# Kernel tuning notes

Hardware: AMD Instinct MI355X
Metric: run time of the kernel (lower is better)

The kernel has to match this reference:

```python
import jax, jax.numpy as jnp
import numpy as np

WS = 8
NUM_HEADS = 4
LOW_THR = 0.2
BN_EPS = 1e-5


def window_partition(x, ws):
    # x: (B, C, H, W) -> (B*nH*nW, C, ws, ws)
    B, C, H, W = x.shape
    x = x.reshape(B, C, H // ws, ws, W // ws, ws)
    return x.transpose(0, 2, 4, 1, 3, 5).reshape(-1, C, ws, ws)


def window_reverse(windows, ws, H, W):
    # (B*nH*nW, C, ws, ws) -> (B, C, H, W)
    Wn, C = windows.shape[0], windows.shape[1]
    B = Wn // ((H // ws) * (W // ws))
    x = windows.reshape(B, H // ws, W // ws, C, ws, ws)
    return x.transpose(0, 3, 1, 4, 2, 5).reshape(B, C, H, W)


def cross_attention(x1, temp, q_w, kv_w, proj_w, proj_b):
    # x1, temp: (Wn, C, h, w); per-window cross attention, windows independent.
    Wn, C, h, w = x1.shape
    N = h * w
    hd = C // NUM_HEADS
    scale = hd ** -0.5
    x1t = x1.reshape(Wn, C, N).transpose(0, 2, 1)    # (Wn, N, C)
    tt = temp.reshape(Wn, C, N).transpose(0, 2, 1)   # (Wn, N, C)
    q = (x1t @ q_w.T).reshape(Wn, N, NUM_HEADS, hd).transpose(0, 2, 1, 3)  # (Wn,H,N,hd)
    kv = (tt @ kv_w.T).reshape(Wn, N, 2, NUM_HEADS, hd).transpose(2, 0, 3, 1, 4)
    k, v = kv[0], kv[1]                               # (Wn,H,N,hd)
    attn = jax.nn.softmax(jnp.einsum('whnd,whmd->whnm', q, k) * scale, axis=-1)
    out = jnp.einsum('whnm,whmd->whnd', attn, v).transpose(0, 2, 1, 3).reshape(Wn, N, C)
    out = out @ proj_w.T + proj_b
    return out.transpose(0, 2, 1).reshape(Wn, C, h, w)


def setup_inputs() -> dict:
    key = jax.random.key(0)
    ks = jax.random.split(key, 8)
    B, C, H, W = 8, 256, 128, 128
    pre_feat = jax.random.normal(ks[0], (B, C, H, W), jnp.float32)
    feat = jax.random.normal(ks[1], (B, C, H, W), jnp.float32)
    pre_feat_mask = jnp.ones((1, 1, H, W), jnp.float32)
    feat_mask = jnp.ones((1, 1, H, W), jnp.float32)
    mask = jax.random.uniform(ks[2], (B, 1, 64, 64), jnp.float32)
    # Linear weights: torch init uses std=0.001; use small std for stable softmax.
    q_w = jax.random.normal(ks[3], (C, C), jnp.float32) * 0.02
    kv_w = jax.random.normal(ks[4], (2 * C, C), jnp.float32) * 0.02
    proj_w = jax.random.normal(ks[5], (C, C), jnp.float32) * 0.02
    proj_b = jnp.zeros((C,), jnp.float32)
    gamma = jnp.ones((C,), jnp.float32)
    beta = jnp.zeros((C,), jnp.float32)
    return {"pre_feat": pre_feat, "pre_feat_mask": pre_feat_mask, "feat": feat,
            "feat_mask": feat_mask, "mask": mask, "q_w": q_w, "kv_w": kv_w,
            "proj_w": proj_w, "proj_b": proj_b, "gamma": gamma, "beta": beta}


def reference(pre_feat, pre_feat_mask, feat, feat_mask, mask,
              q_w, kv_w, proj_w, proj_b, gamma, beta):
    B, C, H, W = feat.shape
    feat = feat * feat_mask
    pre_feat = pre_feat * pre_feat_mask
    # bilinear interpolate mask to (H, W), align_corners=False (half-pixel)
    mask = jax.image.resize(mask, (B, 1, H, W), method='bilinear')
    mask = mask * feat_mask
    feat_p = window_partition(feat, WS)          # (Wn, C, ws, ws)
    pre_p = window_partition(pre_feat, WS)
    mask_p = window_partition(mask, WS)          # (Wn, 1, ws, ws)
    Wn = mask_p.shape[0]
    mask_max = mask_p.reshape(Wn, -1).max(axis=-1)
    keep = mask_max >= LOW_THR                   # (Wn,) bool
    # Windows are independent in the per-window attention, so compute attention
    # over all windows and zero out the non-kept ones (same math as gather/scatter).
    heat_attn = cross_attention(feat_p, pre_p * mask_p, q_w, kv_w, proj_w, proj_b)
    heat_compe = jnp.where(keep[:, None, None, None], heat_attn, 0.0)
    heat_enhance = window_reverse(heat_compe, WS, H, W)
    x = heat_enhance + feat
    # training-mode BatchNorm2d with batch statistics
    mean = x.mean(axis=(0, 2, 3), keepdims=True)
    var = x.var(axis=(0, 2, 3), keepdims=True)
    xhat = (x - mean) * jax.lax.rsqrt(var + BN_EPS)
    return xhat * gamma[None, :, None, None] + beta[None, :, None, None]
```

## Files before the change

### kernel.cpp

```cpp
#include <hip/hip_runtime.h>

typedef unsigned short u16;
typedef unsigned int   u32;
typedef __attribute__((ext_vector_type(8))) short short8;
typedef __attribute__((ext_vector_type(8))) unsigned short u16x8;
typedef __attribute__((ext_vector_type(4))) float floatx4;

__device__ __forceinline__ float bf2f(u16 u) {
  union { u32 i; float f; } v; v.i = ((u32)u) << 16; return v.f;
}
__device__ __forceinline__ u16 f2bf(float f) {
  union { float f; u32 i; } v; v.f = f;
  u32 x = v.i;
  return (u16)((x + 0x7fffu + ((x >> 16) & 1u)) >> 16);
}

__device__ __forceinline__ void gl_lds16(const u16* g, u16* l) {
  __builtin_amdgcn_global_load_lds(
      (const __attribute__((address_space(1))) void*)g,
      (__attribute__((address_space(3))) void*)l, 16, 0, 0);
}

__global__ __launch_bounds__(256) void k_cvtw(const float* __restrict__ qw,
    const float* __restrict__ kvw, const float* __restrict__ pw,
    u16* __restrict__ dst) {
  int i = blockIdx.x * 256 + threadIdx.x;
  float v;
  if (i < 65536)        v = qw[i];
  else if (i < 196608)  v = kvw[i - 65536];
  else                  v = pw[i - 196608];
  dst[i] = f2bf(v);
}

__global__ __launch_bounds__(256) void k_interp(const float* __restrict__ mask,
                                                const float* __restrict__ fmask,
                                                float* __restrict__ E) {
  int idx = blockIdx.x * 256 + threadIdx.x;
  int b = idx >> 14, y = (idx >> 7) & 127, x = idx & 127;
  int jy = y >> 1, jx = x >> 1;
  int y0, y1, x0, x1; float wy0, wx0;
  if (y & 1) { y0 = jy; y1 = jy + 1 > 63 ? 63 : jy + 1; wy0 = 0.75f; }
  else       { y0 = jy - 1 < 0 ? 0 : jy - 1; y1 = jy;    wy0 = 0.25f; }
  if (x & 1) { x0 = jx; x1 = jx + 1 > 63 ? 63 : jx + 1; wx0 = 0.75f; }
  else       { x0 = jx - 1 < 0 ? 0 : jx - 1; x1 = jx;    wx0 = 0.25f; }
  const float* mb = mask + (b << 12);
  float v0 = wx0 * mb[y0*64 + x0] + (1.f - wx0) * mb[y0*64 + x1];
  float v1 = wx0 * mb[y1*64 + x0] + (1.f - wx0) * mb[y1*64 + x1];
  float v  = wy0 * v0 + (1.f - wy0) * v1;
  E[idx] = v * fmask[y*128 + x];
}

__global__ __launch_bounds__(64) void k_keep(const float* __restrict__ E,
                                             int* __restrict__ keepf) {
  int win = blockIdx.x;
  int lane = threadIdx.x;
  int b = win >> 8, wh = (win >> 4) & 15, ww = win & 15;
  int hi = lane >> 3, wi = lane & 7;
  float v = E[(b << 14) + (wh*8 + hi)*128 + ww*8 + wi];
  #pragma unroll
  for (int off = 32; off; off >>= 1) v = fmaxf(v, __shfl_xor(v, off, 64));
  if (lane == 0) keepf[win] = (v >= 0.2f) ? 1 : 0;
}

__global__ __launch_bounds__(256) void k_stage(const float* __restrict__ feat,
    const float* __restrict__ fmask, const float* __restrict__ pre,
    const float* __restrict__ pmask, const float* __restrict__ E,
    u16* __restrict__ Xw, u16* __restrict__ Tw) {
  __shared__ u16 lds[64 * 257];
  int win = blockIdx.x;
  int b = win >> 8, wh = (win >> 4) & 15, ww = win & 15;
  int h0 = wh * 8, w0 = ww * 8;
  int tid = threadIdx.x;
  int hi = tid & 7, cL = tid >> 3;
  int rowoff = (h0 + hi) * 128 + w0;
  float m[8];
  {
    floatx4 a = *(const floatx4*)(fmask + rowoff);
    floatx4 c = *(const floatx4*)(fmask + rowoff + 4);
    #pragma unroll
    for (int j = 0; j < 4; j++) { m[j] = a[j]; m[4 + j] = c[j]; }
  }
  #pragma unroll
  for (int i = 0; i < 8; i++) {
    int c = i * 32 + cL;
    size_t g = (((size_t)(b*256 + c)) << 14) + rowoff;
    floatx4 f0 = *(const floatx4*)(feat + g);
    floatx4 f1 = *(const floatx4*)(feat + g + 4);
    #pragma unroll
    for (int j = 0; j < 4; j++) {
      lds[(hi*8 + j)*257 + c]     = f2bf(f0[j] * m[j]);
      lds[(hi*8 + j + 4)*257 + c] = f2bf(f1[j] * m[4 + j]);
    }
  }
  __syncthreads();
  #pragma unroll
  for (int i = 0; i < 32; i++) {
    int pix = i*2 + (tid >> 7);
    int c = (tid & 127) * 2;
    u32 u = (u32)lds[pix*257 + c] | ((u32)lds[pix*257 + c + 1] << 16);
    *(u32*)(Xw + (((size_t)(win*64 + pix)) << 8) + c) = u;
  }
  __syncthreads();
  {
    floatx4 a = *(const floatx4*)(pmask + rowoff);
    floatx4 c = *(const floatx4*)(pmask + rowoff + 4);
    floatx4 e0 = *(const floatx4*)(E + (b << 14) + rowoff);
    floatx4 e1 = *(const floatx4*)(E + (b << 14) + rowoff + 4);
    #pragma unroll
    for (int j = 0; j < 4; j++) { m[j] = a[j] * e0[j]; m[4 + j] = c[j] * e1[j]; }
  }
  #pragma unroll
  for (int i = 0; i < 8; i++) {
    int c = i * 32 + cL;
    size_t g = (((size_t)(b*256 + c)) << 14) + rowoff;
    floatx4 f0 = *(const floatx4*)(pre + g);
    floatx4 f1 = *(const floatx4*)(pre + g + 4);
    #pragma unroll
    for (int j = 0; j < 4; j++) {
      lds[(hi*8 + j)*257 + c]     = f2bf(f0[j] * m[j]);
      lds[(hi*8 + j + 4)*257 + c] = f2bf(f1[j] * m[4 + j]);
    }
  }
  __syncthreads();
  #pragma unroll
  for (int i = 0; i < 32; i++) {
    int pix = i*2 + (tid >> 7);
    int c = (tid & 127) * 2;
    u32 u = (u32)lds[pix*257 + c] | ((u32)lds[pix*257 + c + 1] << 16);
    *(u32*)(Tw + (((size_t)(win*64 + pix)) << 8) + c) = u;
  }
}

__global__ __launch_bounds__(256) void k_gemm128n(const u16* __restrict__ A,
    const u16* __restrict__ W, const float* __restrict__ bias,
    u16* __restrict__ C) {
  __shared__ u16 As[128 * 32], Ws[128 * 32];
  int bi = blockIdx.x;
  int xcd = bi & 7, t = bi >> 3;
  int y = t & 1, xg = t >> 1;
  int row0 = (xg * 8 + xcd) << 7, col0 = y << 7;
  int wv = threadIdx.x >> 6, lane = threadIdx.x & 63;
  int qq = lane >> 4, l = lane & 15;
  int srow = lane >> 2, skoff = (lane & 3) << 3;
  const u16* Ag = A + (size_t)(row0 + wv*32 + srow) * 256 + skoff;
  const u16* Wg = W + (size_t)(col0 + wv*32 + srow) * 256 + skoff;
  u16* AsW = As + (wv*32) * 32;
  u16* WsW = Ws + (wv*32) * 32;
  int wr = wv >> 1, wc = wv & 1;
  int r0 = wr * 64, c0 = wc * 64;
  floatx4 z = {0.f, 0.f, 0.f, 0.f};
  floatx4 acc[4][4];
  #pragma unroll
  for (int a = 0; a < 4; a++)
    #pragma unroll
    for (int b = 0; b < 4; b++) acc[a][b] = z;
  for (int kb = 0; kb < 256; kb += 32) {
    __syncthreads();
    gl_lds16(Ag + kb,            AsW);
    gl_lds16(Ag + kb + 16*256,   AsW + 16*32);
    gl_lds16(Wg + kb,            WsW);
    gl_lds16(Wg + kb + 16*256,   WsW + 16*32);
    __syncthreads();
    short8 af[4], wf[4];
    #pragma unroll
    for (int tn = 0; tn < 4; tn++)
      af[tn] = *(const short8*)&As[(r0 + tn*16 + l)*32 + qq*8];
    #pragma unroll
    for (int tm = 0; tm < 4; tm++)
      wf[tm] = *(const short8*)&Ws[(c0 + tm*16 + l)*32 + qq*8];
    #pragma unroll
    for (int tn = 0; tn < 4; tn++)
      #pragma unroll
      for (int tm = 0; tm < 4; tm++)
        acc[tn][tm] = __builtin_amdgcn_mfma_f32_16x16x32_bf16(af[tn], wf[tm], acc[tn][tm], 0, 0, 0);
  }
  #pragma unroll
  for (int tm = 0; tm < 4; tm++) {
    int col = col0 + c0 + tm*16 + l;
    float bv = bias ? bias[col] : 0.f;
    #pragma unroll
    for (int tn = 0; tn < 4; tn++) {
      #pragma unroll
      for (int r = 0; r < 4; r++) {
        int row = row0 + r0 + tn*16 + qq*4 + r;
        C[(size_t)row * 256 + col] = f2bf(acc[tn][tm][r] + bv);
      }
    }
  }
}

__global__ __launch_bounds__(256) void k_gemm128kv(const u16* __restrict__ A,
    const u16* __restrict__ W, u16* __restrict__ Kb, u16* __restrict__ Vt) {
  __shared__ u16 As[128 * 32], Ws[128 * 32];
  int bi = blockIdx.x;
  int xcd = bi & 7, t = bi >> 3;
  int y = t & 3, xg = t >> 2;
  int row0 = (xg * 8 + xcd) << 7, col0 = y << 7;
  int wv = threadIdx.x >> 6, lane = threadIdx.x & 63;
  int qq = lane >> 4, l = lane & 15;
  int srow = lane >> 2, skoff = (lane & 3) << 3;
  const u16* Ag = A + (size_t)(row0 + wv*32 + srow) * 256 + skoff;
  const u16* Wg = W + (size_t)(col0 + wv*32 + srow) * 256 + skoff;
  u16* AsW = As + (wv*32) * 32;
  u16* WsW = Ws + (wv*32) * 32;
  int wr = wv >> 1, wc = wv & 1;
  int r0 = wr * 64, c0 = wc * 64;
  floatx4 z = {0.f, 0.f, 0.f, 0.f};
  floatx4 acc[4][4];
  #pragma unroll
  for (int a = 0; a < 4; a++)
    #pragma unroll
    for (int b = 0; b < 4; b++) acc[a][b] = z;
  for (int kb = 0; kb < 256; kb += 32) {
    __syncthreads();
    gl_lds16(Ag + kb,            AsW);
    gl_lds16(Ag + kb + 16*256,   AsW + 16*32);
    gl_lds16(Wg + kb,            WsW);
    gl_lds16(Wg + kb + 16*256,   WsW + 16*32);
    __syncthreads();
    short8 af[4], wf[4];
    #pragma unroll
    for (int tn = 0; tn < 4; tn++)
      af[tn] = *(const short8*)&As[(r0 + tn*16 + l)*32 + qq*8];
    #pragma unroll
    for (int tm = 0; tm < 4; tm++)
      wf[tm] = *(const short8*)&Ws[(c0 + tm*16 + l)*32 + qq*8];
    #pragma unroll
    for (int tn = 0; tn < 4; tn++)
      #pragma unroll
      for (int tm = 0; tm < 4; tm++)
        acc[tn][tm] = __builtin_amdgcn_mfma_f32_16x16x32_bf16(af[tn], wf[tm], acc[tn][tm], 0, 0, 0);
  }
  #pragma unroll
  for (int tm = 0; tm < 4; tm++) {
    int col = col0 + c0 + tm*16 + l;
    #pragma unroll
    for (int tn = 0; tn < 4; tn++) {
      #pragma unroll
      for (int r = 0; r < 4; r++) {
        int row = row0 + r0 + tn*16 + qq*4 + r;
        u16 v = f2bf(acc[tn][tm][r]);
        if (col < 256) {
          Kb[(size_t)row * 256 + col] = v;
        } else {
          int cc = col - 256, hd = cc >> 6, d = cc & 63;
          int wn = row >> 6, mm = row & 63;
          Vt[((size_t)(wn*4 + hd)*64 + d)*64 + mm] = v;
        }
      }
    }
  }
}

__global__ __launch_bounds__(256) void k_attn(const u16* __restrict__ Q,
    const u16* __restrict__ Kb, const u16* __restrict__ Vt,
    u16* __restrict__ O) {
  __shared__ __align__(16) u16 P[4][64 * 72];
  int win = blockIdx.x;
  int head = threadIdx.x >> 6, lane = threadIdx.x & 63;
  int qq = lane >> 4, l = lane & 15;
  const u16* Qh = Q  + (size_t)win * 64 * 256 + head * 64;
  const u16* Kh = Kb + (size_t)win * 64 * 256 + head * 64;
  floatx4 z = {0.f, 0.f, 0.f, 0.f};
  floatx4 s[4][4];
  #pragma unroll
  for (int a = 0; a < 4; a++)
    #pragma unroll
    for (int b = 0; b < 4; b++) s[a][b] = z;
  #pragma unroll
  for (int kb = 0; kb < 64; kb += 32) {
    short8 af[4], bf[4];
    #pragma unroll
    for (int tn = 0; tn < 4; tn++)
      af[tn] = *(const short8*)(Qh + (size_t)(tn*16 + l) * 256 + kb + qq*8);
    #pragma unroll
    for (int tm = 0; tm < 4; tm++)
      bf[tm] = *(const short8*)(Kh + (size_t)(tm*16 + l) * 256 + kb + qq*8);
    #pragma unroll
    for (int tn = 0; tn < 4; tn++)
      #pragma unroll
      for (int tm = 0; tm < 4; tm++)
        s[tn][tm] = __builtin_amdgcn_mfma_f32_16x16x32_bf16(af[tn], bf[tm], s[tn][tm], 0, 0, 0);
  }
  #pragma unroll
  for (int tn = 0; tn < 4; tn++) {
    #pragma unroll
    for (int r = 0; r < 4; r++) {
      float v[4];
      #pragma unroll
      for (int tm = 0; tm < 4; tm++) v[tm] = s[tn][tm][r] * 0.125f;
      float mx = -3.0e38f;
      #pragma unroll
      for (int tm = 0; tm < 4; tm++) mx = fmaxf(mx, v[tm]);
      #pragma unroll
      for (int off = 1; off < 16; off <<= 1) mx = fmaxf(mx, __shfl_xor(mx, off, 64));
      float p0[4], sum = 0.f;
      #pragma unroll
      for (int tm = 0; tm < 4; tm++) { p0[tm] = __expf(v[tm] - mx); sum += p0[tm]; }
      #pragma unroll
      for (int off = 1; off < 16; off <<= 1) sum += __shfl_xor(sum, off, 64);
      float inv = 1.0f / sum;
      int n = tn*16 + qq*4 + r;
      #pragma unroll
      for (int tm = 0; tm < 4; tm++)
        P[head][n*72 + tm*16 + l] = f2bf(p0[tm] * inv);
    }
  }
  __syncthreads();
  floatx4 o[4][4];
  #pragma unroll
  for (int a = 0; a < 4; a++)
    #pragma unroll
    for (int b = 0; b < 4; b++) o[a][b] = z;
  #pragma unroll
  for (int kb = 0; kb < 64; kb += 32) {
    short8 af[4], bf[4];
    #pragma unroll
    for (int tn = 0; tn < 4; tn++)
      af[tn] = *(const short8*)(&P[head][(tn*16 + l)*72 + kb + qq*8]);
    #pragma unroll
    for (int td = 0; td < 4; td++)
      bf[td] = *(const short8*)(Vt + ((size_t)(win*4 + head)*64 + td*16 + l)*64 + kb + qq*8);
    #pragma unroll
    for (int tn = 0; tn < 4; tn++)
      #pragma unroll
      for (int td = 0; td < 4; td++)
        o[tn][td] = __builtin_amdgcn_mfma_f32_16x16x32_bf16(af[tn], bf[td], o[tn][td], 0, 0, 0);
  }
  #pragma unroll
  for (int tn = 0; tn < 4; tn++)
    #pragma unroll
    for (int td = 0; td < 4; td++)
      #pragma unroll
      for (int r = 0; r < 4; r++)
        O[(size_t)(win*64 + tn*16 + qq*4 + r) * 256 + head*64 + td*16 + l] =
            f2bf(o[tn][td][r]);
}

__global__ __launch_bounds__(256) void k_reverse(const u16* __restrict__ heat,
    const int* __restrict__ keepf, const float* __restrict__ feat,
    const float* __restrict__ fmask, float* __restrict__ xbuf,
    float* __restrict__ stats) {
  __shared__ u16 lds[64 * 257];
  int win = blockIdx.x;
  int b = win >> 8, wh = (win >> 4) & 15, ww = win & 15;
  int h0 = wh * 8, w0 = ww * 8;
  int tid = threadIdx.x;
  float kp = keepf[win] ? 1.f : 0.f;
  #pragma unroll
  for (int i = 0; i < 32; i++) {
    int pix = i*2 + (tid >> 7);
    int c = (tid & 127) * 2;
    u32 u = *(const u32*)(heat + (((size_t)(win*64 + pix)) << 8) + c);
    lds[pix*257 + c]     = (u16)(u & 0xffffu);
    lds[pix*257 + c + 1] = (u16)(u >> 16);
  }
  __syncthreads();
  int hi = tid & 7, cL = tid >> 3;
  int rowoff = (h0 + hi) * 128 + w0;
  float m[8];
  {
    floatx4 a = *(const floatx4*)(fmask + rowoff);
    floatx4 c = *(const floatx4*)(fmask + rowoff + 4);
    #pragma unroll
    for (int j = 0; j < 4; j++) { m[j] = a[j]; m[4 + j] = c[j]; }
  }
  #pragma unroll
  for (int i = 0; i < 8; i++) {
    int c = i * 32 + cL;
    size_t goff = (((size_t)(b*256 + c)) << 14) + rowoff;
    floatx4 f0 = *(const floatx4*)(feat + goff);
    floatx4 f1 = *(const floatx4*)(feat + goff + 4);
    floatx4 o0, o1;
    float ls = 0.f, lss = 0.f;
    #pragma unroll
    for (int j = 0; j < 4; j++) {
      o0[j] = kp * bf2f(lds[(hi*8 + j)*257 + c])     + f0[j] * m[j];
      o1[j] = kp * bf2f(lds[(hi*8 + j + 4)*257 + c]) + f1[j] * m[4 + j];
      ls += o0[j] + o1[j];
      lss += o0[j]*o0[j] + o1[j]*o1[j];
    }
    *(floatx4*)(xbuf + goff)     = o0;
    *(floatx4*)(xbuf + goff + 4) = o1;
    #pragma unroll
    for (int off = 1; off < 8; off <<= 1) {
      ls  += __shfl_xor(ls,  off, 64);
      lss += __shfl_xor(lss, off, 64);
    }
    if (hi == 0) {
      atomicAdd(&stats[c],       ls);
      atomicAdd(&stats[256 + c], lss);
    }
  }
}

__global__ void k_scaleshift(const float* __restrict__ stats,
                             const float* __restrict__ gamma,
                             const float* __restrict__ beta,
                             float* __restrict__ scsh) {
  int c = threadIdx.x;
  const float invN = 1.0f / 131072.0f;
  float mean = stats[c] * invN;
  float var  = stats[256 + c] * invN - mean * mean;
  float sc = gamma[c] * rsqrtf(var + 1e-5f);
  scsh[c] = sc;
  scsh[256 + c] = beta[c] - mean * sc;
}

__global__ __launch_bounds__(256) void k_norm(float* __restrict__ xbuf,
                                              const float* __restrict__ scsh) {
  size_t e = ((size_t)blockIdx.x * 256 + threadIdx.x) * 4;
  int c = (int)((e >> 14) & 255);
  float sc = scsh[c], sh = scsh[256 + c];
  floatx4 v4 = *(const floatx4*)(xbuf + e);
  #pragma unroll
  for (int j = 0; j < 4; j++) v4[j] = v4[j] * sc + sh;
  *(floatx4*)(xbuf + e) = v4;
}

extern "C" void kernel_launch(void* const* d_in, const int* in_sizes, int n_in,
                              void* d_out, int out_size, void* d_ws, size_t ws_size,
                              hipStream_t stream) {
  (void)in_sizes; (void)n_in; (void)out_size; (void)ws_size;
  const float* pre    = (const float*)d_in[0];
  const float* pmask  = (const float*)d_in[1];
  const float* feat   = (const float*)d_in[2];
  const float* fmask  = (const float*)d_in[3];
  const float* maskin = (const float*)d_in[4];
  const float* q_w    = (const float*)d_in[5];
  const float* kv_w   = (const float*)d_in[6];
  const float* proj_w = (const float*)d_in[7];
  const float* proj_b = (const float*)d_in[8];
  const float* gamma  = (const float*)d_in[9];
  const float* beta   = (const float*)d_in[10];
  float* out = (float*)d_out;

  const size_t NE = 33554432;
  u16* Xw = (u16*)d_ws;
  u16* Tw = Xw + NE;
  u16* Qb = Tw + NE;
  u16* Kb = Qb + NE;
  u16* Vt = Kb + NE;
  u16* Wb = Vt + NE;
  float* E     = (float*)(Wb + 262144);
  int*   keepf = (int*)(E + 131072);
  float* stats = (float*)(keepf + 2048);
  float* scsh  = stats + 512;

  hipMemsetAsync(stats, 0, 2048, stream);
  k_cvtw<<<1024, 256, 0, stream>>>(q_w, kv_w, proj_w, Wb);
  k_interp<<<512, 256, 0, stream>>>(maskin, fmask, E);
  k_keep<<<2048, 64, 0, stream>>>(E, keepf);
  k_stage<<<2048, 256, 0, stream>>>(feat, fmask, pre, pmask, E, Xw, Tw);
  k_gemm128n<<<2048, 256, 0, stream>>>(Xw, Wb, nullptr, Qb);
  k_gemm128kv<<<4096, 256, 0, stream>>>(Tw, Wb + 65536, Kb, Vt);
  k_attn<<<2048, 256, 0, stream>>>(Qb, Kb, Vt, Xw );
  k_gemm128n<<<2048, 256, 0, stream>>>(Xw , Wb + 196608, proj_b, Tw );
  k_reverse<<<2048, 256, 0, stream>>>(Tw , keepf, feat, fmask,
                                      out , stats);
  k_scaleshift<<<1, 256, 0, stream>>>(stats, gamma, beta, scsh);
  k_norm<<<32768, 256, 0, stream>>>(out, scsh);
}
```

Before: 925.6 us.

## Store KV row-major and transpose V in attention via LDS; swizzle window order

The KV projection now writes K and V together into one row-major buffer instead of scattering V into a transposed layout, which removes the uncoalesced strided stores. The attention kernel stages each head's V tile through per-head shared memory, reads it back transposed into registers, then reuses the same buffer for the softmax probabilities. Because each head uses only its own buffer, the block-wide __syncthreads is dropped. k_stage and k_reverse also remap block index to window so that consecutive blocks fall on different batches, likely to spread memory traffic across XCDs. The costs are extra LDS traffic, scalar transposed LDS reads, and more registers held for V fragments.

```diff
diff --git a/kernel.cpp b/kernel.cpp
--- a/kernel.cpp
+++ b/kernel.cpp
@@ -67,7 +67,8 @@
     const float* __restrict__ pmask, const float* __restrict__ E,
     u16* __restrict__ Xw, u16* __restrict__ Tw) {
   __shared__ u16 lds[64 * 257];
-  int win = blockIdx.x;
+  int bid = blockIdx.x;
+  int win = (bid & 7) * 256 + (bid >> 3);
   int b = win >> 8, wh = (win >> 4) & 15, ww = win & 15;
   int h0 = wh * 8, w0 = ww * 8;
   int tid = threadIdx.x;
@@ -190,7 +191,7 @@
 }
 
 __global__ __launch_bounds__(256) void k_gemm128kv(const u16* __restrict__ A,
-    const u16* __restrict__ W, u16* __restrict__ Kb, u16* __restrict__ Vt) {
+    const u16* __restrict__ W, u16* __restrict__ Cb) {
   __shared__ u16 As[128 * 32], Ws[128 * 32];
   int bi = blockIdx.x;
   int xcd = bi & 7, t = bi >> 3;
@@ -239,28 +240,38 @@
       #pragma unroll
       for (int r = 0; r < 4; r++) {
         int row = row0 + r0 + tn*16 + qq*4 + r;
-        u16 v = f2bf(acc[tn][tm][r]);
-        if (col < 256) {
-          Kb[(size_t)row * 256 + col] = v;
-        } else {
-          int cc = col - 256, hd = cc >> 6, d = cc & 63;
-          int wn = row >> 6, mm = row & 63;
-          Vt[((size_t)(wn*4 + hd)*64 + d)*64 + mm] = v;
-        }
+        Cb[(size_t)row * 512 + col] = f2bf(acc[tn][tm][r]);
       }
     }
   }
 }
 
 __global__ __launch_bounds__(256) void k_attn(const u16* __restrict__ Q,
-    const u16* __restrict__ Kb, const u16* __restrict__ Vt,
-    u16* __restrict__ O) {
-  __shared__ __align__(16) u16 P[4][64 * 72];
+    const u16* __restrict__ KV, u16* __restrict__ O) {
+  __shared__ __align__(16) u16 buf[4][64 * 72];
   int win = blockIdx.x;
   int head = threadIdx.x >> 6, lane = threadIdx.x & 63;
   int qq = lane >> 4, l = lane & 15;
   const u16* Qh = Q  + (size_t)win * 64 * 256 + head * 64;
-  const u16* Kh = Kb + (size_t)win * 64 * 256 + head * 64;
+  const u16* Kh = KV + (size_t)win * 64 * 512 + head * 64;
+  const u16* Vh = Kh + 256;
+  u16* hb = &buf[head][0];
+  {
+    int mg = lane >> 3, dg = lane & 7;
+    #pragma unroll
+    for (int i = 0; i < 8; i++) {
+      int m = i*8 + mg;
+      *(u16x8*)(hb + m*72 + dg*8) = *(const u16x8*)(Vh + (size_t)m*512 + dg*8);
+    }
+  }
+  short8 vf[2][4];
+  #pragma unroll
+  for (int kbh = 0; kbh < 2; kbh++)
+    #pragma unroll
+    for (int td = 0; td < 4; td++)
+      #pragma unroll
+      for (int j = 0; j < 8; j++)
+        ((u16*)&vf[kbh][td])[j] = hb[(kbh*32 + qq*8 + j)*72 + td*16 + l];
   floatx4 z = {0.f, 0.f, 0.f, 0.f};
   floatx4 s[4][4];
   #pragma unroll
@@ -275,7 +286,7 @@
       af[tn] = *(const short8*)(Qh + (size_t)(tn*16 + l) * 256 + kb + qq*8);
     #pragma unroll
     for (int tm = 0; tm < 4; tm++)
-      bf[tm] = *(const short8*)(Kh + (size_t)(tm*16 + l) * 256 + kb + qq*8);
+      bf[tm] = *(const short8*)(Kh + (size_t)(tm*16 + l) * 512 + kb + qq*8);
     #pragma unroll
     for (int tn = 0; tn < 4; tn++)
       #pragma unroll
@@ -303,29 +314,25 @@
       int n = tn*16 + qq*4 + r;
       #pragma unroll
       for (int tm = 0; tm < 4; tm++)
-        P[head][n*72 + tm*16 + l] = f2bf(p0[tm] * inv);
-    }
-  }
-  __syncthreads();
+        hb[n*72 + tm*16 + l] = f2bf(p0[tm] * inv);
+    }
+  }
   floatx4 o[4][4];
   #pragma unroll
   for (int a = 0; a < 4; a++)
     #pragma unroll
     for (int b = 0; b < 4; b++) o[a][b] = z;
   #pragma unroll
-  for (int kb = 0; kb < 64; kb += 32) {
-    short8 af[4], bf[4];
-    #pragma unroll
-    for (int tn = 0; tn < 4; tn++)
-      af[tn] = *(const short8*)(&P[head][(tn*16 + l)*72 + kb + qq*8]);
-    #pragma unroll
-    for (int td = 0; td < 4; td++)
-      bf[td] = *(const short8*)(Vt + ((size_t)(win*4 + head)*64 + td*16 + l)*64 + kb + qq*8);
+  for (int kbh = 0; kbh < 2; kbh++) {
+    short8 af[4];
+    #pragma unroll
+    for (int tn = 0; tn < 4; tn++)
+      af[tn] = *(const short8*)(hb + (tn*16 + l)*72 + kbh*32 + qq*8);
     #pragma unroll
     for (int tn = 0; tn < 4; tn++)
       #pragma unroll
       for (int td = 0; td < 4; td++)
-        o[tn][td] = __builtin_amdgcn_mfma_f32_16x16x32_bf16(af[tn], bf[td], o[tn][td], 0, 0, 0);
+        o[tn][td] = __builtin_amdgcn_mfma_f32_16x16x32_bf16(af[tn], vf[kbh][td], o[tn][td], 0, 0, 0);
   }
   #pragma unroll
   for (int tn = 0; tn < 4; tn++)
@@ -342,7 +349,8 @@
     const float* __restrict__ fmask, float* __restrict__ xbuf,
     float* __restrict__ stats) {
   __shared__ u16 lds[64 * 257];
-  int win = blockIdx.x;
+  int bid = blockIdx.x;
+  int win = (bid & 7) * 256 + (bid >> 3);
   int b = win >> 8, wh = (win >> 4) & 15, ww = win & 15;
   int h0 = wh * 8, w0 = ww * 8;
   int tid = threadIdx.x;
@@ -439,9 +447,8 @@
   u16* Xw = (u16*)d_ws;
   u16* Tw = Xw + NE;
   u16* Qb = Tw + NE;
-  u16* Kb = Qb + NE;
-  u16* Vt = Kb + NE;
-  u16* Wb = Vt + NE;
+  u16* KV = Qb + NE;
+  u16* Wb = KV + 2*NE;
   float* E     = (float*)(Wb + 262144);
   int*   keepf = (int*)(E + 131072);
   float* stats = (float*)(keepf + 2048);
@@ -453,8 +460,8 @@
   k_keep<<<2048, 64, 0, stream>>>(E, keepf);
   k_stage<<<2048, 256, 0, stream>>>(feat, fmask, pre, pmask, E, Xw, Tw);
   k_gemm128n<<<2048, 256, 0, stream>>>(Xw, Wb, nullptr, Qb);
-  k_gemm128kv<<<4096, 256, 0, stream>>>(Tw, Wb + 65536, Kb, Vt);
-  k_attn<<<2048, 256, 0, stream>>>(Qb, Kb, Vt, Xw );
+  k_gemm128kv<<<4096, 256, 0, stream>>>(Tw, Wb + 65536, KV);
+  k_attn<<<2048, 256, 0, stream>>>(Qb, KV, Xw );
   k_gemm128n<<<2048, 256, 0, stream>>>(Xw , Wb + 196608, proj_b, Tw );
   k_reverse<<<2048, 256, 0, stream>>>(Tw , keepf, feat, fmask,
                                       out , stats);
```

Measured after the change: 774.7 us. -16.3%, faster.
